# Kernel tuning notes

Hardware: AMD Instinct MI355X
Metric: run time of the kernel (lower is better)

The kernel has to match this reference:

```python
import jax, jax.numpy as jnp
import numpy as np

Qn, Y, X = 9, 2048, 2048
VUY, PR, ALPHA1, ALPHA01, MUY = 1.4, 0.71, 1.35, 1.05, 0.01
UAX, UAY = 0.0, 0.0
EX_INT = [1, 0, -1, 0, 1, -1, -1, 1, 0]
EY_INT = [0, 1, 0, -1, 1, 1, -1, -1, 0]
EX = jnp.asarray(EX_INT, jnp.float32) + UAX
EY = jnp.asarray(EY_INT, jnp.float32) + UAY
ICV = VUY - 1.0   # 1/Cv
CV = 1.0 / ICV
# streaming shifts: Y_indices = (y - (-ey1)) % Y, X_indices = (x - ex1) % X
# gathering with those indices == jnp.roll(field, (-ey1, ex1))
SHIFTS = [(-EY_INT[q], EX_INT[q]) for q in range(Qn)]


def setup_inputs() -> dict:
    key = jax.random.key(0)
    k1, k2, k3 = jax.random.split(key, 3)
    F = jax.random.uniform(k1, (Qn, Y, X), jnp.float32)
    G = jax.random.uniform(k2, (Qn, Y, X), jnp.float32)
    Feq = jax.random.uniform(k3, (Qn, Y, X), jnp.float32)
    return {"F": F, "G": G, "Feq": Feq}


def reference(F, G, Feq):
    # ---- macroscopic moments ----
    rho = jnp.clip(jnp.sum(F, axis=0), 1e-6)              # (Y, X)
    inv_rho = 1.0 / rho
    ux = jnp.einsum('q,qyx->yx', EX, F) * inv_rho
    uy = jnp.einsum('q,qyx->yx', EY, F) * inv_rho
    E = jnp.sum(G, axis=0) * 0.5 * inv_rho
    # ---- temperature from energy ----
    uu = ux * ux + uy * uy
    T = jnp.clip(ICV * (E - uu * 0.5), 1e-6)
    # ---- Maxwellian heat flux ----
    rhoH2 = 2.0 * rho * (E + T)
    qx = rhoH2 * ux
    qy = rhoH2 * uy
    # ---- G-weights ----
    one_minus_T = 1.0 - T
    w = jnp.concatenate([
        jnp.broadcast_to((one_minus_T * T * 0.5)[None], (4, Y, X)),
        jnp.broadcast_to((T * T * 0.25)[None], (4, Y, X)),
        (one_minus_T * one_minus_T)[None],
    ], axis=0)                                             # (Qn, Y, X)
    # ---- adaptive relaxation times ----
    tau_DL = MUY / (rho * T) + 0.5
    EPS = jnp.mean(jnp.abs(F - Feq) / (Feq + 1e-10), axis=0)
    alpha = jnp.ones_like(EPS)
    alpha = jnp.where(EPS < 0.01, 1.0, alpha)
    alpha = jnp.where(EPS < 0.1, ALPHA01, alpha)
    alpha = jnp.where(EPS < 1.0, ALPHA1, alpha)
    alpha = jnp.where(EPS >= 1.0, jax.lax.stop_gradient(1.0 / tau_DL), alpha)  # .detach()
    tau = alpha * tau_DL
    tauT = 0.5 + (tau - 0.5) / PR
    omega = 1.0 / tau
    omegaT = 1.0 / tauT
    # ---- BGK collision on F + periodic-shift streaming ----
    F_post = F - omega[None] * (F - Feq)
    F_str = jnp.stack([jnp.roll(F_post[q], SHIFTS[q], axis=(0, 1)) for q in range(Qn)], axis=0)
    # pack all moment outputs with the streamed field: (Qn + Qn + 8, Y, X)
    fields = jnp.stack([rho, ux, uy, E, T, qx, qy, omegaT], axis=0)
    return jnp.concatenate([F_str, w, fields], axis=0)
```

## Files before the change

kernel.cpp:

```cpp
#include <hip/hip_runtime.h>

namespace {

constexpr int QN = 9;
constexpr int YD = 2048;
constexpr int XD = 2048;

constexpr float PRc     = 0.71f;
constexpr float ALPHA1c = 1.35f;
constexpr float MUYc    = 0.01f;
constexpr float ICVc    = 1.4f - 1.0f;

__global__ __launch_bounds__(256) void lb_fused(
    const float* __restrict__ Fin,
    const float* __restrict__ Gin,
    const float* __restrict__ Feqin,
    float* __restrict__ out)
{
    constexpr int EXI[QN] = {1, 0, -1, 0, 1, -1, -1, 1, 0};
    constexpr int EYI[QN] = {0, 1, 0, -1, 1, 1, -1, -1, 0};

    const int tid = blockIdx.x * 256 + threadIdx.x;
    const int x0  = (tid & (XD / 4 - 1)) * 4;
    const int y   = tid >> 9;
    const size_t plane = (size_t)YD * XD;
    const size_t base  = (size_t)y * XD + x0;

    float f[QN][4];
    float feq[QN][4];
    float sumG[4] = {0.f, 0.f, 0.f, 0.f};

    #pragma unroll
    for (int q = 0; q < QN; ++q) {
        const float4 fv = *reinterpret_cast<const float4*>(Fin   + q * plane + base);
        const float4 fe = *reinterpret_cast<const float4*>(Feqin + q * plane + base);
        const float4 gv = *reinterpret_cast<const float4*>(Gin   + q * plane + base);
        f[q][0] = fv.x; f[q][1] = fv.y; f[q][2] = fv.z; f[q][3] = fv.w;
        feq[q][0] = fe.x; feq[q][1] = fe.y; feq[q][2] = fe.z; feq[q][3] = fe.w;
        sumG[0] += gv.x; sumG[1] += gv.y; sumG[2] += gv.z; sumG[3] += gv.w;
    }

    float rho[4], ux[4], uy[4], E[4], T[4], qx[4], qy[4], omgT[4], omg[4];
    float wA[4], wB[4], wC[4];

    #pragma unroll
    for (int j = 0; j < 4; ++j) {
        float s = 0.f;
        #pragma unroll
        for (int q = 0; q < QN; ++q) s += f[q][j];
        const float r  = fmaxf(s, 1e-6f);
        const float ir = 1.0f / r;
        const float vx = (f[0][j] - f[2][j] + f[4][j] - f[5][j] - f[6][j] + f[7][j]) * ir;
        const float vy = (f[1][j] - f[3][j] + f[4][j] + f[5][j] - f[6][j] - f[7][j]) * ir;
        const float e  = sumG[j] * 0.5f * ir;
        const float uu = vx * vx + vy * vy;
        const float t  = fmaxf(ICVc * (e - 0.5f * uu), 1e-6f);
        const float rhoH2 = 2.0f * r * (e + t);
        const float one_mt = 1.0f - t;

        float eps = 0.f;
        #pragma unroll
        for (int q = 0; q < QN; ++q)
            eps += fabsf(f[q][j] - feq[q][j]) / (feq[q][j] + 1e-10f);
        eps *= (1.0f / 9.0f);

        const float tau_DL = MUYc / (r * t) + 0.5f;
        const float alpha  = (eps < 1.0f) ? ALPHA1c : (1.0f / tau_DL);
        const float tau    = alpha * tau_DL;
        const float tauT   = 0.5f + (tau - 0.5f) / PRc;

        omg[j]  = 1.0f / tau;
        omgT[j] = 1.0f / tauT;
        rho[j] = r; ux[j] = vx; uy[j] = vy; E[j] = e; T[j] = t;
        qx[j] = rhoH2 * vx; qy[j] = rhoH2 * vy;
        wA[j] = one_mt * t * 0.5f;
        wB[j] = t * t * 0.25f;
        wC[j] = one_mt * one_mt;
    }

    #pragma unroll
    for (int q = 0; q < QN; ++q) {
        const int yp = (y - EYI[q]) & (YD - 1);
        float fp[4];
        #pragma unroll
        for (int j = 0; j < 4; ++j)
            fp[j] = f[q][j] - omg[j] * (f[q][j] - feq[q][j]);
        float* oplane = out + q * plane + (size_t)yp * XD;
        if (EXI[q] == 0) {
            *reinterpret_cast<float4*>(oplane + x0) =
                make_float4(fp[0], fp[1], fp[2], fp[3]);
        } else {
            #pragma unroll
            for (int j = 0; j < 4; ++j) {
                const int xp = (x0 + j + EXI[q]) & (XD - 1);
                oplane[xp] = fp[j];
            }
        }
    }

    auto store4 = [&](int p, const float* v) {
        *reinterpret_cast<float4*>(out + (size_t)p * plane + base) =
            make_float4(v[0], v[1], v[2], v[3]);
    };
    store4(9, wA);  store4(10, wA); store4(11, wA); store4(12, wA);
    store4(13, wB); store4(14, wB); store4(15, wB); store4(16, wB);
    store4(17, wC);
    store4(18, rho); store4(19, ux); store4(20, uy); store4(21, E);
    store4(22, T);   store4(23, qx); store4(24, qy); store4(25, omgT);
}

}

extern "C" void kernel_launch(void* const* d_in, const int* in_sizes, int n_in,
                              void* d_out, int out_size, void* d_ws, size_t ws_size,
                              hipStream_t stream) {
    const float* F   = (const float*)d_in[0];
    const float* G   = (const float*)d_in[1];
    const float* Feq = (const float*)d_in[2];
    float* out = (float*)d_out;

    const int total_threads = (XD / 4) * YD;
    const int block = 256;
    const int grid  = total_threads / block;
    lb_fused<<<grid, block, 0, stream>>>(F, G, Feq, out);
}
```

Measured before the change: 202.9 us.

## Use wavefront shuffles for x-shifted streaming stores plus nontemporal memory ops

Replaces scalar scattered stores for the x-shifted populations with cross-lane shuffles, so each lane writes an aligned float4 and the wavefront edge lanes patch the boundary elements. All global loads and stores become nontemporal, and the divides become hardware reciprocal approximations. The moment stores are moved before the streaming stores, which may also lower register pressure. The risks are small precision differences from rcp and the added shuffle and branch overhead.

After: 204.2 us. About the same (+0.6%).

```diff
diff --git a/kernel.cpp b/kernel.cpp
--- a/kernel.cpp
+++ b/kernel.cpp
@@ -11,6 +11,10 @@
 constexpr float MUYc    = 0.01f;
 constexpr float ICVc    = 1.4f - 1.0f;
 
+typedef float fvec4 __attribute__((ext_vector_type(4)));
+
+__device__ __forceinline__ float rcpf(float x) { return __builtin_amdgcn_rcpf(x); }
+
 __global__ __launch_bounds__(256) void lb_fused(
     const float* __restrict__ Fin,
     const float* __restrict__ Gin,
@@ -20,9 +24,10 @@
     constexpr int EXI[QN] = {1, 0, -1, 0, 1, -1, -1, 1, 0};
     constexpr int EYI[QN] = {0, 1, 0, -1, 1, 1, -1, -1, 0};
 
-    const int tid = blockIdx.x * 256 + threadIdx.x;
-    const int x0  = (tid & (XD / 4 - 1)) * 4;
-    const int y   = tid >> 9;
+    const int tid  = blockIdx.x * 256 + threadIdx.x;
+    const int lane = threadIdx.x & 63;
+    const int x0   = (tid & (XD / 4 - 1)) * 4;
+    const int y    = tid >> 9;
     const size_t plane = (size_t)YD * XD;
     const size_t base  = (size_t)y * XD + x0;
 
@@ -32,81 +37,118 @@
 
     #pragma unroll
     for (int q = 0; q < QN; ++q) {
-        const float4 fv = *reinterpret_cast<const float4*>(Fin   + q * plane + base);
-        const float4 fe = *reinterpret_cast<const float4*>(Feqin + q * plane + base);
-        const float4 gv = *reinterpret_cast<const float4*>(Gin   + q * plane + base);
-        f[q][0] = fv.x; f[q][1] = fv.y; f[q][2] = fv.z; f[q][3] = fv.w;
-        feq[q][0] = fe.x; feq[q][1] = fe.y; feq[q][2] = fe.z; feq[q][3] = fe.w;
-        sumG[0] += gv.x; sumG[1] += gv.y; sumG[2] += gv.z; sumG[3] += gv.w;
+        const fvec4 fv = __builtin_nontemporal_load(
+            reinterpret_cast<const fvec4*>(Fin   + q * plane + base));
+        const fvec4 fe = __builtin_nontemporal_load(
+            reinterpret_cast<const fvec4*>(Feqin + q * plane + base));
+        const fvec4 gv = __builtin_nontemporal_load(
+            reinterpret_cast<const fvec4*>(Gin   + q * plane + base));
+        #pragma unroll
+        for (int j = 0; j < 4; ++j) {
+            f[q][j]   = fv[j];
+            feq[q][j] = fe[j];
+            sumG[j]  += gv[j];
+        }
     }
 
-    float rho[4], ux[4], uy[4], E[4], T[4], qx[4], qy[4], omgT[4], omg[4];
-    float wA[4], wB[4], wC[4];
+    float omg[4];
+    {
+        float rho[4], ux[4], uy[4], E[4], T[4], qx[4], qy[4], omgT[4];
+        float wA[4], wB[4], wC[4];
 
-    #pragma unroll
-    for (int j = 0; j < 4; ++j) {
-        float s = 0.f;
         #pragma unroll
-        for (int q = 0; q < QN; ++q) s += f[q][j];
-        const float r  = fmaxf(s, 1e-6f);
-        const float ir = 1.0f / r;
-        const float vx = (f[0][j] - f[2][j] + f[4][j] - f[5][j] - f[6][j] + f[7][j]) * ir;
-        const float vy = (f[1][j] - f[3][j] + f[4][j] + f[5][j] - f[6][j] - f[7][j]) * ir;
-        const float e  = sumG[j] * 0.5f * ir;
-        const float uu = vx * vx + vy * vy;
-        const float t  = fmaxf(ICVc * (e - 0.5f * uu), 1e-6f);
-        const float rhoH2 = 2.0f * r * (e + t);
-        const float one_mt = 1.0f - t;
+        for (int j = 0; j < 4; ++j) {
+            float s = 0.f;
+            #pragma unroll
+            for (int q = 0; q < QN; ++q) s += f[q][j];
+            const float r  = fmaxf(s, 1e-6f);
+            const float ir = rcpf(r);
+            const float vx = (f[0][j] - f[2][j] + f[4][j] - f[5][j] - f[6][j] + f[7][j]) * ir;
+            const float vy = (f[1][j] - f[3][j] + f[4][j] + f[5][j] - f[6][j] - f[7][j]) * ir;
+            const float e  = sumG[j] * 0.5f * ir;
+            const float uu = vx * vx + vy * vy;
+            const float t  = fmaxf(ICVc * (e - 0.5f * uu), 1e-6f);
+            const float rhoH2 = 2.0f * r * (e + t);
+            const float one_mt = 1.0f - t;
 
-        float eps = 0.f;
-        #pragma unroll
-        for (int q = 0; q < QN; ++q)
-            eps += fabsf(f[q][j] - feq[q][j]) / (feq[q][j] + 1e-10f);
-        eps *= (1.0f / 9.0f);
+            float eps = 0.f;
+            #pragma unroll
+            for (int q = 0; q < QN; ++q)
+                eps += fabsf(f[q][j] - feq[q][j]) * rcpf(feq[q][j] + 1e-10f);
+            eps *= (1.0f / 9.0f);
 
-        const float tau_DL = MUYc / (r * t) + 0.5f;
-        const float alpha  = (eps < 1.0f) ? ALPHA1c : (1.0f / tau_DL);
-        const float tau    = alpha * tau_DL;
-        const float tauT   = 0.5f + (tau - 0.5f) / PRc;
+            const float tau_DL = MUYc * rcpf(r * t) + 0.5f;
+            const float alpha  = (eps < 1.0f) ? ALPHA1c : rcpf(tau_DL);
+            const float tau    = alpha * tau_DL;
+            const float tauT   = 0.5f + (tau - 0.5f) * (1.0f / PRc);
 
-        omg[j]  = 1.0f / tau;
-        omgT[j] = 1.0f / tauT;
-        rho[j] = r; ux[j] = vx; uy[j] = vy; E[j] = e; T[j] = t;
-        qx[j] = rhoH2 * vx; qy[j] = rhoH2 * vy;
-        wA[j] = one_mt * t * 0.5f;
-        wB[j] = t * t * 0.25f;
-        wC[j] = one_mt * one_mt;
+            omg[j]  = rcpf(tau);
+            omgT[j] = rcpf(tauT);
+            rho[j] = r; ux[j] = vx; uy[j] = vy; E[j] = e; T[j] = t;
+            qx[j] = rhoH2 * vx; qy[j] = rhoH2 * vy;
+            wA[j] = one_mt * t * 0.5f;
+            wB[j] = t * t * 0.25f;
+            wC[j] = one_mt * one_mt;
+        }
+
+        auto store4 = [&](int p, const float* v) {
+            fvec4 pv; pv[0] = v[0]; pv[1] = v[1]; pv[2] = v[2]; pv[3] = v[3];
+            __builtin_nontemporal_store(pv,
+                reinterpret_cast<fvec4*>(out + (size_t)p * plane + base));
+        };
+        store4(9, wA);  store4(10, wA); store4(11, wA); store4(12, wA);
+        store4(13, wB); store4(14, wB); store4(15, wB); store4(16, wB);
+        store4(17, wC);
+        store4(18, rho); store4(19, ux); store4(20, uy); store4(21, E);
+        store4(22, T);   store4(23, qx); store4(24, qy); store4(25, omgT);
     }
+
+    const size_t row0 = (size_t)y * XD;
+    const size_t rowm = (size_t)((y - 1) & (YD - 1)) * XD;
+    const size_t rowp = (size_t)((y + 1) & (YD - 1)) * XD;
 
     #pragma unroll
     for (int q = 0; q < QN; ++q) {
-        const int yp = (y - EYI[q]) & (YD - 1);
+        const int ex = EXI[q];
+        const int ey = EYI[q];
+        const size_t rowb = (ey == 0) ? row0 : ((ey == 1) ? rowm : rowp);
         float fp[4];
         #pragma unroll
         for (int j = 0; j < 4; ++j)
             fp[j] = f[q][j] - omg[j] * (f[q][j] - feq[q][j]);
-        float* oplane = out + q * plane + (size_t)yp * XD;
-        if (EXI[q] == 0) {
-            *reinterpret_cast<float4*>(oplane + x0) =
-                make_float4(fp[0], fp[1], fp[2], fp[3]);
+        float* oplane = out + q * plane + rowb;
+
+        if (ex == 0) {
+            fvec4 pv; pv[0] = fp[0]; pv[1] = fp[1]; pv[2] = fp[2]; pv[3] = fp[3];
+            __builtin_nontemporal_store(pv, reinterpret_cast<fvec4*>(oplane + x0));
+        } else if (ex == 1) {
+            const float n0 = __shfl_down(fp[0], 1);
+            const float n1 = __shfl_down(fp[1], 1);
+            const float n2 = __shfl_down(fp[2], 1);
+            fvec4 pv; pv[0] = fp[3]; pv[1] = n0; pv[2] = n1; pv[3] = n2;
+            if (lane != 63)
+                __builtin_nontemporal_store(pv, reinterpret_cast<fvec4*>(oplane + x0 + 4));
+            if (lane == 0) {
+                oplane[x0 + 1] = fp[0];
+                oplane[x0 + 2] = fp[1];
+                oplane[x0 + 3] = fp[2];
+            }
+            if (lane == 63)
+                oplane[(x0 + 4) & (XD - 1)] = fp[3];
         } else {
-            #pragma unroll
-            for (int j = 0; j < 4; ++j) {
-                const int xp = (x0 + j + EXI[q]) & (XD - 1);
-                oplane[xp] = fp[j];
+            const float n0 = __shfl_down(fp[0], 1);
+            fvec4 pv; pv[0] = fp[1]; pv[1] = fp[2]; pv[2] = fp[3]; pv[3] = n0;
+            if (lane != 63)
+                __builtin_nontemporal_store(pv, reinterpret_cast<fvec4*>(oplane + x0));
+            if (lane == 63) {
+                oplane[x0]     = fp[1];
+                oplane[x0 + 1] = fp[2];
+                oplane[x0 + 2] = fp[3];
             }
+            if (lane == 0)
+                oplane[(x0 - 1) & (XD - 1)] = fp[0];
         }
     }
-
-    auto store4 = [&](int p, const float* v) {
-        *reinterpret_cast<float4*>(out + (size_t)p * plane + base) =
-            make_float4(v[0], v[1], v[2], v[3]);
-    };
-    store4(9, wA);  store4(10, wA); store4(11, wA); store4(12, wA);
-    store4(13, wB); store4(14, wB); store4(15, wB); store4(16, wB);
-    store4(17, wC);
-    store4(18, rho); store4(19, ux); store4(20, uy); store4(21, E);
-    store4(22, T);   store4(23, qx); store4(24, qy); store4(25, omgT);
 }
 
 }
```
